# Kernel optimization log

Measured on AMD Instinct MI355X. Metric: run time of the kernel, lower is better.

The kernel has to match this reference:

```python
import jax, jax.numpy as jnp
import numpy as np

N_NODES = 50000
N_EDGES = 800000
N_HIDDEN = 64
N_LAYER = 3
IN_DIM = 4


def setup_inputs() -> dict:
    key = jax.random.key(0)
    ks = jax.random.split(key, 10)
    x = jax.random.normal(ks[0], (N_NODES, IN_DIM), dtype=jnp.float32)
    edge_index = jax.random.randint(ks[1], (2, N_EDGES), 0, N_NODES, dtype=jnp.int64)
    # Glorot-style params matching pyg GCNConv (lin has no bias; conv adds bias after aggregation)
    def glorot(k, fan_in, fan_out):
        s = jnp.sqrt(6.0 / (fan_in + fan_out))
        return jax.random.uniform(k, (fan_in, fan_out), jnp.float32, -s, s)
    W_in = glorot(ks[2], IN_DIM, N_HIDDEN)
    b_in = jnp.zeros((N_HIDDEN,), jnp.float32)
    W_h = jnp.stack([glorot(jax.random.fold_in(ks[3], i), N_HIDDEN, N_HIDDEN) for i in range(N_LAYER)])
    b_h = jnp.zeros((N_LAYER, N_HIDDEN), jnp.float32)
    W_out = glorot(ks[4], N_HIDDEN, 1)
    b_out = jnp.zeros((1,), jnp.float32)
    return {"x": x, "edge_index": edge_index, "W_in": W_in, "b_in": b_in,
            "W_h": W_h, "b_h": b_h, "W_out": W_out, "b_out": b_out}


def _gcn_norm(edge_index, n_nodes):
    # add self-loops, compute symmetric norm D^{-1/2} (A+I) D^{-1/2}
    loop = jnp.arange(n_nodes, dtype=edge_index.dtype)
    src = jnp.concatenate([edge_index[0], loop])
    dst = jnp.concatenate([edge_index[1], loop])
    deg = jax.ops.segment_sum(jnp.ones_like(dst, dtype=jnp.float32), dst, num_segments=n_nodes)
    dinv = jax.lax.rsqrt(deg)  # deg >= 1 due to self-loops
    norm = dinv[src] * dinv[dst]
    return src, dst, norm


def _gcn_conv(x, W, b, src, dst, norm, n_nodes):
    h = x @ W                                   # [N, out]
    msg = h[src] * norm[:, None]                # gather + scale, [E+N, out]
    out = jax.ops.segment_sum(msg, dst, num_segments=n_nodes)  # scatter-add
    return out + b


def reference(x, edge_index, W_in, b_in, W_h, b_h, W_out, b_out):
    n = x.shape[0]
    src, dst, norm = _gcn_norm(edge_index, n)
    h = jax.nn.relu(_gcn_conv(x, W_in, b_in, src, dst, norm, n))
    for i in range(W_h.shape[0]):
        h = jax.nn.relu(_gcn_conv(h, W_h[i], b_h[i], src, dst, norm, n))
    return _gcn_conv(h, W_out, b_out, src, dst, norm, n)
```

## Files before the change

kernel.cpp:

```cpp
#include <hip/hip_runtime.h>
#include <hip/hip_bf16.h>


#define TPB 256
#define EPT 8
#define CHUNK (TPB * EPT)
typedef __hip_bfloat16 bf16;
#define B2F __bfloat162float

__global__ void k_zero_b(int* __restrict__ bktcnt) {
    bktcnt[threadIdx.x] = 0;
}

__global__ __launch_bounds__(TPB) void k_bktcnt(
    const int* __restrict__ dst, int* __restrict__ bktcnt, int E, int n) {
    __shared__ int h[256];
    int tid = threadIdx.x;
    h[tid] = 0;
    __syncthreads();
    int e0 = blockIdx.x * CHUNK;
#pragma unroll
    for (int u = 0; u < EPT; ++u) {
        int e = e0 + u * TPB + tid;
        if (e < E) {
            int d = dst[e];
            if ((unsigned)d < (unsigned)n) atomicAdd(&h[d >> 8], 1);
        }
    }
    __syncthreads();
    if (h[tid]) atomicAdd(&bktcnt[tid], h[tid]);
}

__global__ void k_bktscan(const int* __restrict__ bktcnt, int* __restrict__ bktbase,
                          int* __restrict__ bcur) {
    __shared__ int s[256];
    int t = threadIdx.x;
    int v = bktcnt[t];
    s[t] = v;
    __syncthreads();
    for (int off = 1; off < 256; off <<= 1) {
        int u = (t >= off) ? s[t - off] : 0;
        __syncthreads();
        s[t] += u;
        __syncthreads();
    }
    int excl = s[t] - v;
    bktbase[t] = excl;
    bcur[t] = excl;
    if (t == 255) bktbase[256] = s[t];
}

__global__ __launch_bounds__(TPB) void k_bin(
    const int* __restrict__ src, const int* __restrict__ dst,
    int* __restrict__ bcur, unsigned* __restrict__ staging, int E, int n) {
    __shared__ int hcnt[256];
    __shared__ int hbase[256];
    int tid = threadIdx.x;
    int e0 = blockIdx.x * CHUNK;
    hcnt[tid] = 0;
    __syncthreads();

    int eb[EPT];
    unsigned rec[EPT];
#pragma unroll
    for (int u = 0; u < EPT; ++u) {
        int e = e0 + u * TPB + tid;
        eb[u] = -1;
        if (e < E) {
            int d = dst[e], s = src[e];
            if ((unsigned)d < (unsigned)n && (unsigned)s < (unsigned)n) {
                eb[u] = d >> 8;
                rec[u] = (unsigned)s | ((unsigned)(d & 255) << 16);
                atomicAdd(&hcnt[eb[u]], 1);
            }
        }
    }
    __syncthreads();
    int c = hcnt[tid];
    hbase[tid] = (c > 0) ? atomicAdd(&bcur[tid], c) : 0;
    hcnt[tid] = 0;
    __syncthreads();
#pragma unroll
    for (int u = 0; u < EPT; ++u) {
        if (eb[u] >= 0) {
            int r = atomicAdd(&hcnt[eb[u]], 1);
            int pos = hbase[eb[u]] + r;
            if ((unsigned)pos < (unsigned)E) staging[pos] = rec[u];
        }
    }
}

__global__ __launch_bounds__(TPB) void k_unbin2(
    const unsigned* __restrict__ staging, const int* __restrict__ bktbase,
    int* __restrict__ row_start, float* __restrict__ dinv,
    unsigned short* __restrict__ bucket, int E, int n) {
    __shared__ int cnt[256];
    __shared__ int scn[256];
    __shared__ int cur[256];
    int b = blockIdx.x, tid = threadIdx.x;
    int lo = bktbase[b], hi = bktbase[b + 1];
    lo = max(0, min(lo, E)); hi = max(lo, min(hi, E));

    cnt[tid] = 0;
    __syncthreads();
    for (int i = lo + tid; i < hi; i += TPB)
        atomicAdd(&cnt[(staging[i] >> 16) & 255], 1);
    __syncthreads();

    int v = cnt[tid];
    scn[tid] = v;
    __syncthreads();
    for (int off = 1; off < 256; off <<= 1) {
        int u = (tid >= off) ? scn[tid - off] : 0;
        __syncthreads();
        scn[tid] += u;
        __syncthreads();
    }
    int excl = scn[tid] - v;
    int base = min(lo + excl, E);
    cur[tid] = base;
    int d = (b << 8) + tid;
    if (d < n) {
        row_start[d] = base;
        dinv[d] = rsqrtf((float)v + 1.0f);
        if (d == n - 1) row_start[n] = min(base + v, E);
    }
    __syncthreads();

    for (int i = lo + tid; i < hi; i += TPB) {
        unsigned r = staging[i];
        int t = (r >> 16) & 255;
        int pos = atomicAdd(&cur[t], 1);
        if ((unsigned)pos < (unsigned)E) bucket[pos] = (unsigned short)(r & 0xffffu);
    }
}

__global__ void k_mm_in(const float* __restrict__ x, const float* __restrict__ W,
                        const float* __restrict__ dinv, bf16* __restrict__ g, int n) {
    int t = blockIdx.x * blockDim.x + threadIdx.x;
    if (t >= n * 64) return;
    int i = t >> 6, j = t & 63;
    float acc = 0.f;
#pragma unroll
    for (int k = 0; k < 4; ++k) acc = fmaf(x[i * 4 + k], W[k * 64 + j], acc);
    g[t] = __float2bfloat16(acc * dinv[i]);
}

__device__ __forceinline__ void acc_oct(float* a, uint4 w) {
    a[0] += __uint_as_float(w.x << 16);
    a[1] += __uint_as_float(w.x & 0xffff0000u);
    a[2] += __uint_as_float(w.y << 16);
    a[3] += __uint_as_float(w.y & 0xffff0000u);
    a[4] += __uint_as_float(w.z << 16);
    a[5] += __uint_as_float(w.z & 0xffff0000u);
    a[6] += __uint_as_float(w.w << 16);
    a[7] += __uint_as_float(w.w & 0xffff0000u);
}

__device__ __forceinline__ void agg_row_oct(const bf16* __restrict__ g,
                                            const unsigned short* __restrict__ bucket,
                                            int k0, int k1, int d, float* __restrict__ sVp,
                                            int lane, unsigned nm1, unsigned Em1) {
    int grp = lane >> 3, i = lane & 7;
    float a[8] = {0.f, 0.f, 0.f, 0.f, 0.f, 0.f, 0.f, 0.f};
    if (grp == 0) {
        uint4 w = *(const uint4*)(g + (size_t)d * 64 + 8 * i);
        acc_oct(a, w);
    }
    for (int base = k0; base < k1; base += 64) {
        int cnt = min(64, k1 - base);
        int rec = bucket[min((unsigned)(base + lane), Em1)];
        int k = 0;
        for (; k + 16 <= cnt; k += 16) {
            unsigned s0 = min((unsigned)__shfl(rec, k + grp), nm1);
            unsigned s1 = min((unsigned)__shfl(rec, k + 8 + grp), nm1);
            uint4 w0 = *(const uint4*)(g + (size_t)s0 * 64 + 8 * i);
            uint4 w1 = *(const uint4*)(g + (size_t)s1 * 64 + 8 * i);
            acc_oct(a, w0);
            acc_oct(a, w1);
        }
        for (; k < cnt; k += 8) {
            int e = k + grp;
            unsigned s = min((unsigned)__shfl(rec, min(e, 63)), nm1);
            uint4 w = *(const uint4*)(g + (size_t)s * 64 + 8 * i);
            if (e < cnt) acc_oct(a, w);
        }
    }
    float4* row = (float4*)(sVp + grp * 64);
    row[2 * i + 0] = make_float4(a[0], a[1], a[2], a[3]);
    row[2 * i + 1] = make_float4(a[4], a[5], a[6], a[7]);
}

__global__ __launch_bounds__(TPB) void k_gconv(
    const bf16* __restrict__ gIn, const float* __restrict__ dinv,
    const int* __restrict__ row_start, const unsigned short* __restrict__ bucket,
    const float* __restrict__ bias, const float* __restrict__ W,
    bf16* __restrict__ gOut, int n, int E) {
    __shared__ float sVp[4][8 * 64];
    int tid = threadIdx.x;
    int r = tid >> 6, j = tid & 63;
    int d = blockIdx.x * 4 + r;
    if (d >= n) return;
    float dd = dinv[d];
    int k0 = row_start[d], k1 = row_start[d + 1];
    k1 = min(k1, E); k0 = max(min(k0, k1), 0);
    agg_row_oct(gIn, bucket, k0, k1, d, sVp[r], j, (unsigned)(n - 1), (unsigned)(E - 1));
    float v = 0.f;
#pragma unroll
    for (int gq = 0; gq < 8; ++gq) v += sVp[r][gq * 64 + j];
    float a = fmaxf(fmaf(dd, v, bias[j]), 0.f);
    sVp[r][j] = a;
    const float4* ap = (const float4*)&sVp[r][0];
    float acc0 = 0.f, acc1 = 0.f, acc2 = 0.f, acc3 = 0.f;
#pragma unroll
    for (int k4 = 0; k4 < 16; ++k4) {
        float4 a4 = ap[k4];
        acc0 = fmaf(a4.x, W[(4 * k4 + 0) * 64 + j], acc0);
        acc1 = fmaf(a4.y, W[(4 * k4 + 1) * 64 + j], acc1);
        acc2 = fmaf(a4.z, W[(4 * k4 + 2) * 64 + j], acc2);
        acc3 = fmaf(a4.w, W[(4 * k4 + 3) * 64 + j], acc3);
    }
    float acc = (acc0 + acc1) + (acc2 + acc3);
    gOut[(size_t)d * 64 + j] = __float2bfloat16(acc * dd);
}

__global__ __launch_bounds__(TPB) void k_gconv_z(
    const bf16* __restrict__ gIn, const float* __restrict__ dinv,
    const int* __restrict__ row_start, const unsigned short* __restrict__ bucket,
    const float* __restrict__ bias, const float* __restrict__ Wout,
    float* __restrict__ zg, int n, int E) {
    __shared__ float sVp[4][8 * 64];
    int tid = threadIdx.x;
    int r = tid >> 6, j = tid & 63;
    int d = blockIdx.x * 4 + r;
    if (d >= n) return;
    float dd = dinv[d];
    int k0 = row_start[d], k1 = row_start[d + 1];
    k1 = min(k1, E); k0 = max(min(k0, k1), 0);
    agg_row_oct(gIn, bucket, k0, k1, d, sVp[r], j, (unsigned)(n - 1), (unsigned)(E - 1));
    float v = 0.f;
#pragma unroll
    for (int gq = 0; gq < 8; ++gq) v += sVp[r][gq * 64 + j];
    float a = fmaxf(fmaf(dd, v, bias[j]), 0.f) * Wout[j];
#pragma unroll
    for (int off = 32; off > 0; off >>= 1) a += __shfl_down(a, off);
    if (j == 0) zg[d] = a * dd;
}

__global__ __launch_bounds__(TPB) void k_out(
    const float* __restrict__ zg, const float* __restrict__ dinv,
    const int* __restrict__ row_start, const unsigned short* __restrict__ bucket,
    const float* __restrict__ b_out, float* __restrict__ out, int n, int E) {
    int t = blockIdx.x * blockDim.x + threadIdx.x;
    int d = t >> 6, lane = t & 63;
    if (d >= n) return;
    int k0 = row_start[d], k1 = row_start[d + 1];
    k1 = min(k1, E); k0 = max(min(k0, k1), 0);
    unsigned nm1 = (unsigned)(n - 1);
    float v = 0.f;
    for (int k = k0 + lane; k < k1; k += 64) {
        unsigned s = min((unsigned)bucket[k], nm1);
        v += zg[s];
    }
#pragma unroll
    for (int off = 32; off > 0; off >>= 1) v += __shfl_down(v, off);
    if (lane == 0) out[d] = fmaf(zg[d] + v, dinv[d], b_out[0]);
}

extern "C" void kernel_launch(void* const* d_in, const int* in_sizes, int n_in,
                              void* d_out, int out_size, void* d_ws, size_t ws_size,
                              hipStream_t stream) {
    const float* x     = (const float*)d_in[0];
    const int*   ei    = (const int*)d_in[1];
    const float* W_in  = (const float*)d_in[2];
    const float* b_in  = (const float*)d_in[3];
    const float* W_h   = (const float*)d_in[4];
    const float* b_h   = (const float*)d_in[5];
    const float* W_out = (const float*)d_in[6];
    const float* b_out = (const float*)d_in[7];
    float* out = (float*)d_out;

    int N = in_sizes[0] / 4;
    int E = in_sizes[1] / 2;
    const int* src = ei;
    const int* dst = ei + E;

    char* ws = (char*)d_ws;
    bf16* gA               = (bf16*)ws;           ws += (size_t)N * 64 * 2;
    bf16* gB               = (bf16*)ws;           ws += (size_t)N * 64 * 2;
    unsigned short* bucket = (unsigned short*)ws; ws += (size_t)E * 2;
    unsigned* staging      = (unsigned*)ws;       ws += (size_t)E * 4;
    int*  row_start        = (int*)ws;            ws += (size_t)(N + 1) * 4;
    float* dinv            = (float*)ws;          ws += (size_t)N * 4;
    float* zg              = (float*)ws;          ws += (size_t)N * 4;
    int*  bktcnt           = (int*)ws;            ws += 256 * 4;
    int*  bktbase          = (int*)ws;            ws += 257 * 4;
    int*  bcur             = (int*)ws;

    int B   = (N + 255) >> 8;
    int gNF = (N * 64 + TPB - 1) / TPB;
    int gN4 = (N + 3) / 4;
    int gBin = (E + CHUNK - 1) / CHUNK;

    k_zero_b<<<1, 256, 0, stream>>>(bktcnt);
    k_bktcnt<<<gBin, TPB, 0, stream>>>(dst, bktcnt, E, N);
    k_bktscan<<<1, 256, 0, stream>>>(bktcnt, bktbase, bcur);
    k_bin<<<gBin, TPB, 0, stream>>>(src, dst, bcur, staging, E, N);
    k_unbin2<<<B, TPB, 0, stream>>>(staging, bktbase, row_start, dinv, bucket, E, N);

    k_mm_in<<<gNF, TPB, 0, stream>>>(x, W_in, dinv, gA, N);
    k_gconv<<<gN4, TPB, 0, stream>>>(gA, dinv, row_start, bucket, b_in, W_h, gB, N, E);
    k_gconv<<<gN4, TPB, 0, stream>>>(gB, dinv, row_start, bucket, b_h, W_h + 4096, gA, N, E);
    k_gconv<<<gN4, TPB, 0, stream>>>(gA, dinv, row_start, bucket, b_h + 64, W_h + 8192, gB, N, E);
    k_gconv_z<<<gN4, TPB, 0, stream>>>(gB, dinv, row_start, bucket, b_h + 128, W_out, zg, N, E);
    k_out<<<gN4, TPB, 0, stream>>>(zg, dinv, row_start, bucket, b_out, out, N, E);
}
```

Measured before the change: 261.7 us.

## Fuse bucket scan into count kernel, use shuffle reductions, stage weights in LDS

Merges the bucket prefix scan into the bucket-count kernel using a last-block atomic ticket, removing one launch. The per-row aggregation now reduces the eight partial groups with cross-lane shuffles instead of writing them to shared memory and summing. The hidden conv kernel caches the 64x64 weight in LDS and processes two rows per wave to amortize that load. The final conv kernel computes the bias/ReLU/output-weight dot product per lane group with vector loads. The 16KB LDS per block and the fewer, longer waves may reduce occupancy and latency hiding for the gather.

```diff
diff --git a/kernel.cpp b/kernel.cpp
--- a/kernel.cpp
+++ b/kernel.cpp
@@ -8,13 +8,16 @@
 typedef __hip_bfloat16 bf16;
 #define B2F __bfloat162float
 
-__global__ void k_zero_b(int* __restrict__ bktcnt) {
+__global__ void k_zero_b(int* __restrict__ bktcnt, int* __restrict__ ticket) {
     bktcnt[threadIdx.x] = 0;
+    if (threadIdx.x == 0) *ticket = 0;
 }
 
 __global__ __launch_bounds__(TPB) void k_bktcnt(
-    const int* __restrict__ dst, int* __restrict__ bktcnt, int E, int n) {
+    const int* __restrict__ dst, int* __restrict__ bktcnt, int* __restrict__ ticket,
+    int* __restrict__ bktbase, int* __restrict__ bcur, int E, int n) {
     __shared__ int h[256];
+    __shared__ int lastFlag;
     int tid = threadIdx.x;
     h[tid] = 0;
     __syncthreads();
@@ -29,25 +32,24 @@
     }
     __syncthreads();
     if (h[tid]) atomicAdd(&bktcnt[tid], h[tid]);
-}
-
-__global__ void k_bktscan(const int* __restrict__ bktcnt, int* __restrict__ bktbase,
-                          int* __restrict__ bcur) {
-    __shared__ int s[256];
-    int t = threadIdx.x;
-    int v = bktcnt[t];
-    s[t] = v;
+    __threadfence();
+    __syncthreads();
+    if (tid == 0) lastFlag = (atomicAdd(ticket, 1) == (int)gridDim.x - 1);
+    __syncthreads();
+    if (!lastFlag) return;
+    int v = atomicAdd(&bktcnt[tid], 0);
+    h[tid] = v;
     __syncthreads();
     for (int off = 1; off < 256; off <<= 1) {
-        int u = (t >= off) ? s[t - off] : 0;
+        int u2 = (tid >= off) ? h[tid - off] : 0;
         __syncthreads();
-        s[t] += u;
+        h[tid] += u2;
         __syncthreads();
     }
-    int excl = s[t] - v;
-    bktbase[t] = excl;
-    bcur[t] = excl;
-    if (t == 255) bktbase[256] = s[t];
+    int excl = h[tid] - v;
+    bktbase[tid] = excl;
+    bcur[tid] = excl;
+    if (tid == 255) bktbase[256] = h[tid];
 }
 
 __global__ __launch_bounds__(TPB) void k_bin(
@@ -157,12 +159,13 @@
     a[7] += __uint_as_float(w.w & 0xffff0000u);
 }
 
-__device__ __forceinline__ void agg_row_oct(const bf16* __restrict__ g,
-                                            const unsigned short* __restrict__ bucket,
-                                            int k0, int k1, int d, float* __restrict__ sVp,
-                                            int lane, unsigned nm1, unsigned Em1) {
+__device__ __forceinline__ void agg_oct(const bf16* __restrict__ g,
+                                        const unsigned short* __restrict__ bucket,
+                                        int k0, int k1, int d, float* __restrict__ a,
+                                        int lane, unsigned nm1, unsigned Em1) {
     int grp = lane >> 3, i = lane & 7;
-    float a[8] = {0.f, 0.f, 0.f, 0.f, 0.f, 0.f, 0.f, 0.f};
+#pragma unroll
+    for (int m = 0; m < 8; ++m) a[m] = 0.f;
     if (grp == 0) {
         uint4 w = *(const uint4*)(g + (size_t)d * 64 + 8 * i);
         acc_oct(a, w);
@@ -186,9 +189,6 @@
             if (e < cnt) acc_oct(a, w);
         }
     }
-    float4* row = (float4*)(sVp + grp * 64);
-    row[2 * i + 0] = make_float4(a[0], a[1], a[2], a[3]);
-    row[2 * i + 1] = make_float4(a[4], a[5], a[6], a[7]);
 }
 
 __global__ __launch_bounds__(TPB) void k_gconv(
@@ -196,7 +196,70 @@
     const int* __restrict__ row_start, const unsigned short* __restrict__ bucket,
     const float* __restrict__ bias, const float* __restrict__ W,
     bf16* __restrict__ gOut, int n, int E) {
-    __shared__ float sVp[4][8 * 64];
+    __shared__ float sW[4096];
+    __shared__ float sAct[4][64];
+    int tid = threadIdx.x;
+    const float4* W4 = (const float4*)W;
+    float4* sW4 = (float4*)sW;
+#pragma unroll
+    for (int t = 0; t < 4; ++t) sW4[tid + t * 256] = W4[tid + t * 256];
+    __syncthreads();
+
+    int r = tid >> 6, j = tid & 63;
+    int grp = j >> 3, i = j & 7;
+    int d0 = blockIdx.x * 8 + r * 2;
+    if (d0 >= n) return;
+    unsigned nm1 = (unsigned)(n - 1), Em1 = (unsigned)(E - 1);
+
+    for (int q = 0; q < 2; ++q) {
+        int d = d0 + q;
+        if (d >= n) break;
+        float dd = dinv[d];
+        int k0 = row_start[d], k1 = row_start[d + 1];
+        k1 = min(k1, E); k0 = max(min(k0, k1), 0);
+        float a[8];
+        agg_oct(gIn, bucket, k0, k1, d, a, j, nm1, Em1);
+#pragma unroll
+        for (int m = 0; m < 8; ++m) {
+            a[m] += __shfl_xor(a[m], 8);
+            a[m] += __shfl_xor(a[m], 16);
+            a[m] += __shfl_xor(a[m], 32);
+        }
+        if (grp == 0) {
+            const float4* b4 = (const float4*)bias;
+            float4 bA = b4[2 * i], bB = b4[2 * i + 1];
+            float4 r0, r1;
+            r0.x = fmaxf(fmaf(dd, a[0], bA.x), 0.f);
+            r0.y = fmaxf(fmaf(dd, a[1], bA.y), 0.f);
+            r0.z = fmaxf(fmaf(dd, a[2], bA.z), 0.f);
+            r0.w = fmaxf(fmaf(dd, a[3], bA.w), 0.f);
+            r1.x = fmaxf(fmaf(dd, a[4], bB.x), 0.f);
+            r1.y = fmaxf(fmaf(dd, a[5], bB.y), 0.f);
+            r1.z = fmaxf(fmaf(dd, a[6], bB.z), 0.f);
+            r1.w = fmaxf(fmaf(dd, a[7], bB.w), 0.f);
+            float4* arow = (float4*)&sAct[r][8 * i];
+            arow[0] = r0; arow[1] = r1;
+        }
+        const float4* ap = (const float4*)&sAct[r][0];
+        float acc0 = 0.f, acc1 = 0.f, acc2 = 0.f, acc3 = 0.f;
+#pragma unroll
+        for (int k4 = 0; k4 < 16; ++k4) {
+            float4 a4 = ap[k4];
+            acc0 = fmaf(a4.x, sW[(4 * k4 + 0) * 64 + j], acc0);
+            acc1 = fmaf(a4.y, sW[(4 * k4 + 1) * 64 + j], acc1);
+            acc2 = fmaf(a4.z, sW[(4 * k4 + 2) * 64 + j], acc2);
+            acc3 = fmaf(a4.w, sW[(4 * k4 + 3) * 64 + j], acc3);
+        }
+        float acc = (acc0 + acc1) + (acc2 + acc3);
+        gOut[(size_t)d * 64 + j] = __float2bfloat16(acc * dd);
+    }
+}
+
+__global__ __launch_bounds__(TPB) void k_gconv_z(
+    const bf16* __restrict__ gIn, const float* __restrict__ dinv,
+    const int* __restrict__ row_start, const unsigned short* __restrict__ bucket,
+    const float* __restrict__ bias, const float* __restrict__ Wout,
+    float* __restrict__ zg, int n, int E) {
     int tid = threadIdx.x;
     int r = tid >> 6, j = tid & 63;
     int d = blockIdx.x * 4 + r;
@@ -204,47 +267,31 @@
     float dd = dinv[d];
     int k0 = row_start[d], k1 = row_start[d + 1];
     k1 = min(k1, E); k0 = max(min(k0, k1), 0);
-    agg_row_oct(gIn, bucket, k0, k1, d, sVp[r], j, (unsigned)(n - 1), (unsigned)(E - 1));
-    float v = 0.f;
-#pragma unroll
-    for (int gq = 0; gq < 8; ++gq) v += sVp[r][gq * 64 + j];
-    float a = fmaxf(fmaf(dd, v, bias[j]), 0.f);
-    sVp[r][j] = a;
-    const float4* ap = (const float4*)&sVp[r][0];
-    float acc0 = 0.f, acc1 = 0.f, acc2 = 0.f, acc3 = 0.f;
-#pragma unroll
-    for (int k4 = 0; k4 < 16; ++k4) {
-        float4 a4 = ap[k4];
-        acc0 = fmaf(a4.x, W[(4 * k4 + 0) * 64 + j], acc0);
-        acc1 = fmaf(a4.y, W[(4 * k4 + 1) * 64 + j], acc1);
-        acc2 = fmaf(a4.z, W[(4 * k4 + 2) * 64 + j], acc2);
-        acc3 = fmaf(a4.w, W[(4 * k4 + 3) * 64 + j], acc3);
-    }
-    float acc = (acc0 + acc1) + (acc2 + acc3);
-    gOut[(size_t)d * 64 + j] = __float2bfloat16(acc * dd);
-}
-
-__global__ __launch_bounds__(TPB) void k_gconv_z(
-    const bf16* __restrict__ gIn, const float* __restrict__ dinv,
-    const int* __restrict__ row_start, const unsigned short* __restrict__ bucket,
-    const float* __restrict__ bias, const float* __restrict__ Wout,
-    float* __restrict__ zg, int n, int E) {
-    __shared__ float sVp[4][8 * 64];
-    int tid = threadIdx.x;
-    int r = tid >> 6, j = tid & 63;
-    int d = blockIdx.x * 4 + r;
-    if (d >= n) return;
-    float dd = dinv[d];
-    int k0 = row_start[d], k1 = row_start[d + 1];
-    k1 = min(k1, E); k0 = max(min(k0, k1), 0);
-    agg_row_oct(gIn, bucket, k0, k1, d, sVp[r], j, (unsigned)(n - 1), (unsigned)(E - 1));
-    float v = 0.f;
-#pragma unroll
-    for (int gq = 0; gq < 8; ++gq) v += sVp[r][gq * 64 + j];
-    float a = fmaxf(fmaf(dd, v, bias[j]), 0.f) * Wout[j];
-#pragma unroll
-    for (int off = 32; off > 0; off >>= 1) a += __shfl_down(a, off);
-    if (j == 0) zg[d] = a * dd;
+    float a[8];
+    agg_oct(gIn, bucket, k0, k1, d, a, j, (unsigned)(n - 1), (unsigned)(E - 1));
+#pragma unroll
+    for (int m = 0; m < 8; ++m) {
+        a[m] += __shfl_xor(a[m], 8);
+        a[m] += __shfl_xor(a[m], 16);
+        a[m] += __shfl_xor(a[m], 32);
+    }
+    int i = j & 7;
+    const float4* b4 = (const float4*)bias;
+    const float4* w4 = (const float4*)Wout;
+    float4 bA = b4[2 * i], bB = b4[2 * i + 1];
+    float4 wA = w4[2 * i], wB = w4[2 * i + 1];
+    float p = fmaxf(fmaf(dd, a[0], bA.x), 0.f) * wA.x
+            + fmaxf(fmaf(dd, a[1], bA.y), 0.f) * wA.y
+            + fmaxf(fmaf(dd, a[2], bA.z), 0.f) * wA.z
+            + fmaxf(fmaf(dd, a[3], bA.w), 0.f) * wA.w
+            + fmaxf(fmaf(dd, a[4], bB.x), 0.f) * wB.x
+            + fmaxf(fmaf(dd, a[5], bB.y), 0.f) * wB.y
+            + fmaxf(fmaf(dd, a[6], bB.z), 0.f) * wB.z
+            + fmaxf(fmaf(dd, a[7], bB.w), 0.f) * wB.w;
+    p += __shfl_xor(p, 1);
+    p += __shfl_xor(p, 2);
+    p += __shfl_xor(p, 4);
+    if (j == 0) zg[d] = p * dd;
 }
 
 __global__ __launch_bounds__(TPB) void k_out(
@@ -294,24 +341,25 @@
     float* dinv            = (float*)ws;          ws += (size_t)N * 4;
     float* zg              = (float*)ws;          ws += (size_t)N * 4;
     int*  bktcnt           = (int*)ws;            ws += 256 * 4;
+    int*  ticket           = (int*)ws;            ws += 4;
     int*  bktbase          = (int*)ws;            ws += 257 * 4;
     int*  bcur             = (int*)ws;
 
     int B   = (N + 255) >> 8;
     int gNF = (N * 64 + TPB - 1) / TPB;
     int gN4 = (N + 3) / 4;
+    int gN8 = (N + 7) / 8;
     int gBin = (E + CHUNK - 1) / CHUNK;
 
-    k_zero_b<<<1, 256, 0, stream>>>(bktcnt);
-    k_bktcnt<<<gBin, TPB, 0, stream>>>(dst, bktcnt, E, N);
-    k_bktscan<<<1, 256, 0, stream>>>(bktcnt, bktbase, bcur);
+    k_zero_b<<<1, 256, 0, stream>>>(bktcnt, ticket);
+    k_bktcnt<<<gBin, TPB, 0, stream>>>(dst, bktcnt, ticket, bktbase, bcur, E, N);
     k_bin<<<gBin, TPB, 0, stream>>>(src, dst, bcur, staging, E, N);
     k_unbin2<<<B, TPB, 0, stream>>>(staging, bktbase, row_start, dinv, bucket, E, N);
 
     k_mm_in<<<gNF, TPB, 0, stream>>>(x, W_in, dinv, gA, N);
-    k_gconv<<<gN4, TPB, 0, stream>>>(gA, dinv, row_start, bucket, b_in, W_h, gB, N, E);
-    k_gconv<<<gN4, TPB, 0, stream>>>(gB, dinv, row_start, bucket, b_h, W_h + 4096, gA, N, E);
-    k_gconv<<<gN4, TPB, 0, stream>>>(gA, dinv, row_start, bucket, b_h + 64, W_h + 8192, gB, N, E);
+    k_gconv<<<gN8, TPB, 0, stream>>>(gA, dinv, row_start, bucket, b_in, W_h, gB, N, E);
+    k_gconv<<<gN8, TPB, 0, stream>>>(gB, dinv, row_start, bucket, b_h, W_h + 4096, gA, N, E);
+    k_gconv<<<gN8, TPB, 0, stream>>>(gA, dinv, row_start, bucket, b_h + 64, W_h + 8192, gB, N, E);
     k_gconv_z<<<gN4, TPB, 0, stream>>>(gB, dinv, row_start, bucket, b_h + 128, W_out, zg, N, E);
     k_out<<<gN4, TPB, 0, stream>>>(zg, dinv, row_start, bucket, b_out, out, N, E);
 }
```

Result: slower. 322.1 us (+23.1%).
